# Optimization experiments

Measured on AMD Instinct MI355X. Metric: run time of the kernel, lower is better.

Reference implementation:

```python
import jax, jax.numpy as jnp
import numpy as np

B, N, R = 8, 1024, 8192
D_IN, REL_D = 32, 1
NF_P, NF_R, NF_E, D_OUT = 128, 128, 128, 3
PSTEP = 3


def setup_inputs() -> dict:
    key = jax.random.key(0)
    ks = jax.random.split(key, 26)
    state = jax.random.normal(ks[0], (B, N, D_IN), dtype=jnp.float32)
    # Rr/Rs are one-hot selection matrices [B, N, R]: column j selects the
    # receiver/sender particle of relation j.
    recv = jax.random.randint(ks[1], (B, R), 0, N)
    send = jax.random.randint(ks[2], (B, R), 0, N)
    Rr = jnp.transpose(jax.nn.one_hot(recv, N, dtype=jnp.float32), (0, 2, 1))
    Rs = jnp.transpose(jax.nn.one_hot(send, N, dtype=jnp.float32), (0, 2, 1))
    Ra = jax.random.normal(ks[3], (B, R, REL_D), dtype=jnp.float32)

    def lin(k, i, o):
        kw, kb = jax.random.split(k)
        return (0.02 * jax.random.normal(kw, (i, o), dtype=jnp.float32),
                0.02 * jax.random.normal(kb, (o,), dtype=jnp.float32))

    pe_w0, pe_b0 = lin(ks[4], D_IN, NF_P)
    pe_w1, pe_b1 = lin(ks[5], NF_P, NF_E)
    re_w0, re_b0 = lin(ks[6], 2 * D_IN + REL_D, NF_R)
    re_w1, re_b1 = lin(ks[7], NF_R, NF_R)
    re_w2, re_b2 = lin(ks[8], NF_R, NF_R)
    rp_w, rp_b = lin(ks[9], NF_R + 2 * NF_E, NF_E)   # relation_propagator
    pp_w, pp_b = lin(ks[10], 2 * NF_E, NF_E)          # particle_propagator
    pr_w0, pr_b0 = lin(ks[11], NF_E, NF_E)            # particle_predictor
    pr_w1, pr_b1 = lin(ks[12], NF_E, D_OUT)
    return dict(state=state, Rr=Rr, Rs=Rs, Ra=Ra, pstep=PSTEP,
                pe_w0=pe_w0, pe_b0=pe_b0, pe_w1=pe_w1, pe_b1=pe_b1,
                re_w0=re_w0, re_b0=re_b0, re_w1=re_w1, re_b1=re_b1,
                re_w2=re_w2, re_b2=re_b2, rp_w=rp_w, rp_b=rp_b,
                pp_w=pp_w, pp_b=pp_b, pr_w0=pr_w0, pr_b0=pr_b0,
                pr_w1=pr_w1, pr_b1=pr_b1)


def reference(state, Rr, Rs, Ra, pstep,
              pe_w0, pe_b0, pe_w1, pe_b1,
              re_w0, re_b0, re_w1, re_b1, re_w2, re_b2,
              rp_w, rp_b, pp_w, pp_b,
              pr_w0, pr_b0, pr_w1, pr_b1):
    relu = jax.nn.relu
    # gather particle states into relation slots: Rr^T @ state -> [B, R, D]
    state_r = jnp.einsum('bnr,bnd->brd', Rr, state)
    state_s = jnp.einsum('bnr,bnd->brd', Rs, state)
    # particle encoder: Linear-ReLU-Linear-ReLU
    particle_encode = relu(relu(state @ pe_w0 + pe_b0) @ pe_w1 + pe_b1)  # [B,N,NF_E]
    # relation encoder: 3-layer MLP with ReLU after each layer
    rel_in = jnp.concatenate([state_r, state_s, Ra], axis=2)
    h = relu(rel_in @ re_w0 + re_b0)
    h = relu(h @ re_w1 + re_b1)
    relation_encode = relu(h @ re_w2 + re_b2)  # [B,R,NF_R]

    particle_effect = jnp.zeros((B, N, NF_E), dtype=state.dtype)
    for _ in range(pstep):
        effect_r = jnp.einsum('bnr,bne->bre', Rr, particle_effect)  # gather
        effect_s = jnp.einsum('bnr,bne->bre', Rs, particle_effect)
        rel_x = jnp.concatenate([relation_encode, effect_r, effect_s], axis=2)
        relation_effect = relu(rel_x @ rp_w + rp_b)  # [B,R,NF_E]
        # scatter-add relation effects back to receiver particles
        effect_agg = jnp.einsum('bnr,bre->bne', Rr, relation_effect)
        part_x = jnp.concatenate([particle_encode, effect_agg], axis=2)
        # residual particle propagator: relu(linear(x) + prev_effect)
        particle_effect = relu(part_x @ pp_w + pp_b + particle_effect)
    pred = relu(particle_effect @ pr_w0 + pr_b0) @ pr_w1 + pr_b1  # [B,N,D_OUT]
    return pred
```

## Files before the change

### kernel.cpp

```cpp
#include <hip/hip_runtime.h>

#define NB 8
#define NP 1024
#define NR 8192

typedef unsigned short u16;
typedef __attribute__((ext_vector_type(8))) short bf16x8;
typedef __attribute__((ext_vector_type(4))) float f32x4;
typedef __attribute__((ext_vector_type(4))) unsigned int u32x4;

#define MFMA __builtin_amdgcn_mfma_f32_16x16x32_bf16

static __device__ __forceinline__ float bf2f(u16 u) {
    union { unsigned int i; float f; } v; v.i = ((unsigned int)u) << 16; return v.f;
}
static __device__ __forceinline__ unsigned int f2bf(float f) {
    union { float fv; unsigned int i; } v; v.fv = f;
    unsigned int r = v.i + 0x7FFFu + ((v.i >> 16) & 1u);
    return r >> 16;
}
static __device__ __forceinline__ unsigned int pack2(float a, float b) {
    return f2bf(a) | (f2bf(b) << 16);
}
static __device__ __forceinline__ void unpk8(uint4 v, float* o) {
    o[0] = bf2f((u16)(v.x & 0xFFFF)); o[1] = bf2f((u16)(v.x >> 16));
    o[2] = bf2f((u16)(v.y & 0xFFFF)); o[3] = bf2f((u16)(v.y >> 16));
    o[4] = bf2f((u16)(v.z & 0xFFFF)); o[5] = bf2f((u16)(v.z >> 16));
    o[6] = bf2f((u16)(v.w & 0xFFFF)); o[7] = bf2f((u16)(v.w >> 16));
}

template<int KC>
static __device__ __forceinline__ void load_wfrag(
    const bf16x8* __restrict__ fb, bf16x8 (&wf)[KC][2], int tid)
{
    #pragma unroll
    for (int kc = 0; kc < KC; ++kc)
      #pragma unroll
      for (int nt = 0; nt < 2; ++nt)
        wf[kc][nt] = fb[(kc*2 + nt)*256 + tid];
}

template<int MT, int KC, int LDA>
static __device__ __forceinline__ void mfma_compute(
    const u16* xlds, const bf16x8 (&wf)[KC][2], f32x4 (&acc)[MT][2],
    int l16, int quad)
{
    #pragma unroll
    for (int kc = 0; kc < KC; ++kc) {
        bf16x8 a[MT];
        #pragma unroll
        for (int mt = 0; mt < MT; ++mt)
            a[mt] = *(const bf16x8*)(xlds + (mt*16 + l16)*LDA + kc*32 + quad*8);
        #pragma unroll
        for (int mt = 0; mt < MT; ++mt) {
            acc[mt][0] = MFMA(a[mt], wf[kc][0], acc[mt][0], 0, 0, 0);
            acc[mt][1] = MFMA(a[mt], wf[kc][1], acc[mt][1], 0, 0, 0);
        }
    }
}

template<int MT>
static __device__ __forceinline__ void zero_acc(f32x4 (&acc)[MT][2]) {
    #pragma unroll
    for (int mt = 0; mt < MT; ++mt)
      #pragma unroll
      for (int nt = 0; nt < 2; ++nt)
        acc[mt][nt] = f32x4{0.f, 0.f, 0.f, 0.f};
}

template<int MT, int LDA>
static __device__ __forceinline__ void store_c_lds(
    u16* xlds, const f32x4 (&acc)[MT][2], const float* __restrict__ bias,
    int wave, int quad, int l16, int coloff = 0)
{
    #pragma unroll
    for (int mt = 0; mt < MT; ++mt)
      #pragma unroll
      for (int nt = 0; nt < 2; ++nt) {
        int col = wave*32 + nt*16 + l16;
        float bv = bias[col];
        #pragma unroll
        for (int rg = 0; rg < 4; ++rg)
            xlds[(mt*16 + quad*4 + rg)*LDA + coloff + col] =
                (u16)f2bf(fmaxf(acc[mt][nt][rg] + bv, 0.f));
      }
}

template<int MT, bool RELU>
static __device__ __forceinline__ void store_c_glob(
    u16* __restrict__ out, long row0, const f32x4 (&acc)[MT][2],
    const float* __restrict__ bias, int wave, int quad, int l16)
{
    #pragma unroll
    for (int mt = 0; mt < MT; ++mt)
      #pragma unroll
      for (int nt = 0; nt < 2; ++nt) {
        int col = wave*32 + nt*16 + l16;
        float bv = bias[col];
        #pragma unroll
        for (int rg = 0; rg < 4; ++rg) {
            long r = row0 + mt*16 + quad*4 + rg;
            float v = acc[mt][nt][rg] + bv;
            if (RELU) v = fmaxf(v, 0.f);
            out[r*128 + col] = (u16)f2bf(v);
        }
      }
}

__global__ __launch_bounds__(256) void k_idxprep(
    const u32x4* __restrict__ Rr4, const u32x4* __restrict__ Rs4,
    u16* __restrict__ recv, u16* __restrict__ send,
    const float* __restrict__ w0, const float* __restrict__ w1,
    const float* __restrict__ w2, const float* __restrict__ w3,
    const float* __restrict__ w4, const float* __restrict__ w5,
    const float* __restrict__ w6, const float* __restrict__ w7,
    bf16x8* __restrict__ wfrag,
    const float* __restrict__ state, const float* __restrict__ pe_b0,
    const float* __restrict__ pe_b1, u16* __restrict__ penc)
{
    constexpr int LDA = 136;
    __shared__ __align__(16) u16 xlds[64 * LDA];
    int tid = threadIdx.x;
    const int wave = tid >> 6, quad = (tid >> 4) & 3, l16 = tid & 15;

    if (blockIdx.x < 8) {
        const float* W; int KC, kv, off;
        switch (blockIdx.x) {
            case 0:  W = w0; KC = 3;  kv = 65;  off = 0;  break;
            case 1:  W = w1; KC = 4;  kv = 128; off = 6;  break;
            case 2:  W = w2; KC = 4;  kv = 128; off = 14; break;
            case 3:  W = w3; KC = 1;  kv = 32;  off = 22; break;
            case 4:  W = w4; KC = 4;  kv = 128; off = 24; break;
            case 5:  W = w5; KC = 12; kv = 384; off = 32; break;
            case 6:  W = w6; KC = 8;  kv = 256; off = 56; break;
            default: W = w7; KC = 4;  kv = 128; off = 72; break;
        }
        for (int kc = 0; kc < KC; ++kc)
          for (int nt = 0; nt < 2; ++nt) {
            bf16x8 f;
            #pragma unroll
            for (int j = 0; j < 8; ++j) {
                int k = kc*32 + quad*8 + j;
                f[j] = (k < kv) ? (short)f2bf(W[k*128 + wave*32 + nt*16 + l16]) : (short)0;
            }
            wfrag[(off + kc*2 + nt)*256 + tid] = f;
          }
        return;
    }

    if (blockIdx.x < 136) {
        const long row0 = (long)(blockIdx.x - 8) * 64;
        for (int idx = tid; idx < 64 * 8; idx += 256) {
            int r = idx >> 3, c = idx & 7;
            float4 v = *(const float4*)(state + (row0 + r)*32 + c*4);
            uint2 o; o.x = pack2(v.x, v.y); o.y = pack2(v.z, v.w);
            *(uint2*)(xlds + r*LDA + c*4) = o;
        }
        __syncthreads();
        f32x4 acc[4][2];
        zero_acc<4>(acc);
        {
            bf16x8 wf[1][2];
            #pragma unroll
            for (int nt = 0; nt < 2; ++nt)
              #pragma unroll
              for (int j = 0; j < 8; ++j) {
                int k = quad*8 + j;
                wf[0][nt][j] = (short)f2bf(w3[k*128 + wave*32 + nt*16 + l16]);
              }
            mfma_compute<4, 1, LDA>(xlds, wf, acc, l16, quad);
        }
        __syncthreads();
        store_c_lds<4, LDA>(xlds, acc, pe_b0, wave, quad, l16);
        __syncthreads();
        zero_acc<4>(acc);
        {
            bf16x8 wf[4][2];
            #pragma unroll
            for (int kc = 0; kc < 4; ++kc)
              #pragma unroll
              for (int nt = 0; nt < 2; ++nt)
                #pragma unroll
                for (int j = 0; j < 8; ++j) {
                    int k = kc*32 + quad*8 + j;
                    wf[kc][nt][j] = (short)f2bf(w4[k*128 + wave*32 + nt*16 + l16]);
                }
            mfma_compute<4, 4, LDA>(xlds, wf, acc, l16, quad);
        }
        store_c_glob<4, true>(penc, row0, acc, pe_b1, wave, quad, l16);
        return;
    }

    int sid = blockIdx.x - 136;
    int mat = sid & 1;
    const u32x4* src = mat ? Rs4 : Rr4;
    u16* dst = mat ? send : recv;
    long base = (long)(sid >> 1) * 2048 + tid;
    u32x4 v[8];
    #pragma unroll
    for (int k = 0; k < 8; ++k)
        v[k] = __builtin_nontemporal_load(src + base + k*256);
    #pragma unroll
    for (int k = 0; k < 8; ++k) {
        long i = base + k*256;
        int c4 = (int)(i & 2047), n = (int)((i >> 11) & 1023), b = (int)(i >> 21);
        int o = b * NR + c4 * 4;
        if (v[k][0]) dst[o + 0] = (u16)n;
        if (v[k][1]) dst[o + 1] = (u16)n;
        if (v[k][2]) dst[o + 2] = (u16)n;
        if (v[k][3]) dst[o + 3] = (u16)n;
    }
}

__global__ __launch_bounds__(256) void k_csrenc(
    const float* __restrict__ state, const float* __restrict__ Ra,
    const u16* __restrict__ recv, const u16* __restrict__ send,
    int* __restrict__ row_ptr, unsigned int* __restrict__ pidx,
    const bf16x8* __restrict__ f_re0, const float* __restrict__ re_b0,
    const bf16x8* __restrict__ f_re1, const float* __restrict__ re_b1,
    const bf16x8* __restrict__ f_re2, const float* __restrict__ re_b2,
    const bf16x8* __restrict__ f_rpP, const float* __restrict__ rp_b,
    u16* __restrict__ bufP)
{
    constexpr int LDA = 136;
    __shared__ __align__(16) u16 xlds[64 * LDA];
    __shared__ int cur[NP];
    __shared__ int wsum[4];
    const int tid = threadIdx.x;

    if (blockIdx.x < 8) {
        const int b = blockIdx.x;
        for (int i = tid; i < NP; i += 256) cur[i] = 0;
        __syncthreads();
        int pv[32];
        #pragma unroll
        for (int k = 0; k < 32; ++k) {
            pv[k] = recv[b * NR + k * 256 + tid] & 1023;
            atomicAdd(&cur[pv[k]], 1);
        }
        __syncthreads();
        int4 c4v = ((const int4*)cur)[tid];
        int s = c4v.x + c4v.y + c4v.z + c4v.w;
        int si = s;
        #pragma unroll
        for (int off = 1; off < 64; off <<= 1) {
            int u = __shfl_up(si, off);
            if ((tid & 63) >= off) si += u;
        }
        if ((tid & 63) == 63) wsum[tid >> 6] = si;
        __syncthreads();
        if (tid == 0) {
            int a0 = 0;
            #pragma unroll
            for (int i = 0; i < 4; ++i) { int w = wsum[i]; wsum[i] = a0; a0 += w; }
        }
        __syncthreads();
        int base = si - s + wsum[tid >> 6];
        int e0 = base, e1 = base + c4v.x, e2 = e1 + c4v.y, e3 = e2 + c4v.z;
        int* rp = row_ptr + b * (NP + 1);
        rp[tid*4 + 0] = e0; rp[tid*4 + 1] = e1;
        rp[tid*4 + 2] = e2; rp[tid*4 + 3] = e3;
        cur[tid*4 + 0] = e0; cur[tid*4 + 1] = e1;
        cur[tid*4 + 2] = e2; cur[tid*4 + 3] = e3;
        if (tid == 255) rp[NP] = e3 + c4v.w;
        __syncthreads();
        #pragma unroll
        for (int k = 0; k < 32; ++k) {
            int r = k * 256 + tid;
            int j = atomicAdd(&cur[pv[k]], 1) & 8191;
            pidx[b * NR + j] = (unsigned int)(r & 8191)
                             | ((unsigned int)(send[b * NR + r] & 1023) << 16);
        }
        return;
    }

    const int wave = tid >> 6, quad = (tid >> 4) & 3, l16 = tid & 15;
    f32x4 acc[4][2];
    const int row0 = (blockIdx.x - 8) * 64;
    const int b = row0 >> 13;
    {
        int r = tid >> 2, tt = tid & 3;
        int rel = row0 + r;
        u16* dst = xlds + r * LDA;
        int ri = recv[rel] & 1023;
        int si = send[rel] & 1023;
        const float* rrow = state + ((long)(b*NP + ri)) * 32;
        const float* srow = state + ((long)(b*NP + si)) * 32;
        float4 a0 = *(const float4*)(rrow + tt*8);
        float4 a1 = *(const float4*)(rrow + tt*8 + 4);
        uint4 o;
        o.x = pack2(a0.x, a0.y); o.y = pack2(a0.z, a0.w);
        o.z = pack2(a1.x, a1.y); o.w = pack2(a1.z, a1.w);
        *(uint4*)(dst + tt*8) = o;
        float4 s0 = *(const float4*)(srow + tt*8);
        float4 s1 = *(const float4*)(srow + tt*8 + 4);
        o.x = pack2(s0.x, s0.y); o.y = pack2(s0.z, s0.w);
        o.z = pack2(s1.x, s1.y); o.w = pack2(s1.z, s1.w);
        *(uint4*)(dst + 32 + tt*8) = o;
        if (tt == 3) {
            uint4 z = make_uint4(0, 0, 0, 0);
            *(uint4*)(dst + 64) = z; *(uint4*)(dst + 72) = z;
            *(uint4*)(dst + 80) = z; *(uint4*)(dst + 88) = z;
            dst[64] = (u16)f2bf(Ra[rel]);
        }
    }
    __syncthreads();
    zero_acc<4>(acc);
    {
        bf16x8 wf[3][2];
        load_wfrag<3>(f_re0, wf, tid);
        mfma_compute<4, 3, LDA>(xlds, wf, acc, l16, quad);
    }
    __syncthreads();
    store_c_lds<4, LDA>(xlds, acc, re_b0, wave, quad, l16);
    __syncthreads();
    zero_acc<4>(acc);
    {
        bf16x8 wf[4][2];
        load_wfrag<4>(f_re1, wf, tid);
        mfma_compute<4, 4, LDA>(xlds, wf, acc, l16, quad);
    }
    __syncthreads();
    store_c_lds<4, LDA>(xlds, acc, re_b1, wave, quad, l16);
    __syncthreads();
    zero_acc<4>(acc);
    {
        bf16x8 wf[4][2];
        load_wfrag<4>(f_re2, wf, tid);
        mfma_compute<4, 4, LDA>(xlds, wf, acc, l16, quad);
    }
    __syncthreads();
    store_c_lds<4, LDA>(xlds, acc, re_b2, wave, quad, l16);
    __syncthreads();
    zero_acc<4>(acc);
    {
        bf16x8 wf[4][2];
        load_wfrag<4>(f_rpP, wf, tid);
        mfma_compute<4, 4, LDA>(xlds, wf, acc, l16, quad);
    }
    #pragma unroll
    for (int mt = 0; mt < 4; ++mt)
      #pragma unroll
      for (int nt = 0; nt < 2; ++nt) {
        int col = wave*32 + nt*16 + l16;
        float bv = rp_b[col];
        #pragma unroll
        for (int rg = 0; rg < 4; ++rg) {
            int rl = mt*16 + quad*4 + rg;
            bufP[((long)(row0 + rl))*128 + col] = (u16)f2bf(acc[mt][nt][rg] + bv);
        }
      }
}

template<bool STEP1, bool MAKEUV, bool LAST>
__global__ __launch_bounds__(256) void k_pp(
    const u16* __restrict__ penc, const u16* __restrict__ bufP,
    const u16* __restrict__ UV_in, u16* __restrict__ UV_out,
    const int* __restrict__ row_ptr, const unsigned int* __restrict__ pidx,
    const bf16x8* __restrict__ f_pp, const float* __restrict__ pp_b,
    const bf16x8* __restrict__ f_U, const bf16x8* __restrict__ f_V,
    const bf16x8* __restrict__ f_pr0, const float* __restrict__ pr_b0,
    const float* __restrict__ pr_w1, const float* __restrict__ pr_b1,
    float* __restrict__ peff32_io, float* __restrict__ out)
{
    constexpr int LDA = 264;
    __shared__ __align__(16) u16 xlds[32 * LDA];
    const int tid = threadIdx.x;
    const int wave = tid >> 6, quad = (tid >> 4) & 3, l16 = tid & 15;
    const long row0 = (long)blockIdx.x * 32;

    for (int idx = tid; idx < 512; idx += 256) {
        int r = idx >> 4, c = idx & 15;
        *(uint4*)(xlds + r*LDA + c*8) = *(const uint4*)(penc + (row0 + r)*128 + c*8);
    }
    {
        int pp = tid >> 3;
        int cq = tid & 7;
        int gp = (int)row0 + pp;
        int b = gp >> 10, pl = gp & 1023;
        const int* rp = row_ptr + b * (NP + 1);
        int s0 = rp[pl], e0 = rp[pl + 1];
        const unsigned int* pidxb = pidx + b * NR;
        const u16* bufPb = bufP + (long)b * NR * 128;
        float a[16];
        #pragma unroll
        for (int t = 0; t < 16; ++t) a[t] = 0.f;
        float uv[16];
        if (!STEP1) {
            const u16* ur = UV_in + ((long)gp)*256 + cq*16;
            unpk8(*(const uint4*)ur, uv);
            unpk8(*(const uint4*)(ur + 8), uv + 8);
        }
        const u16* uvb = UV_in + ((long)(b*NP))*256 + 128 + cq*16;
        for (int jb = s0; jb < e0; jb += 4) {
            int m = e0 - jb; if (m > 4) m = 4;
            unsigned int ids[4];
            #pragma unroll
            for (int t = 0; t < 4; ++t) {
                int j = jb + t; if (j > e0 - 1) j = e0 - 1;
                ids[t] = pidxb[j];
            }
            uint4 P0[4], P1[4], V0[4], V1[4];
            #pragma unroll
            for (int t = 0; t < 4; ++t) {
                const u16* prow = bufPb + ((long)(ids[t] & 8191u))*128 + cq*16;
                P0[t] = *(const uint4*)prow;
                P1[t] = *(const uint4*)(prow + 8);
                if (!STEP1) {
                    const u16* vrow = uvb + (long)((ids[t] >> 16) & 1023u)*256;
                    V0[t] = *(const uint4*)vrow;
                    V1[t] = *(const uint4*)(vrow + 8);
                }
            }
            #pragma unroll
            for (int t = 0; t < 4; ++t) {
                if (t < m) {
                    float pv[16];
                    unpk8(P0[t], pv); unpk8(P1[t], pv + 8);
                    if (STEP1) {
                        #pragma unroll
                        for (int e = 0; e < 16; ++e) a[e] += fmaxf(pv[e], 0.f);
                    } else {
                        float vv[16];
                        unpk8(V0[t], vv); unpk8(V1[t], vv + 8);
                        #pragma unroll
                        for (int e = 0; e < 16; ++e)
                            a[e] += fmaxf(pv[e] + uv[e] + vv[e], 0.f);
                    }
                }
            }
        }
        u16* dst = xlds + pp*LDA + 128 + cq*16;
        uint4 o;
        o.x = pack2(a[0], a[1]);   o.y = pack2(a[2], a[3]);
        o.z = pack2(a[4], a[5]);   o.w = pack2(a[6], a[7]);
        *(uint4*)dst = o;
        o.x = pack2(a[8], a[9]);   o.y = pack2(a[10], a[11]);
        o.z = pack2(a[12], a[13]); o.w = pack2(a[14], a[15]);
        *(uint4*)(dst + 8) = o;
    }
    __syncthreads();

    f32x4 acc[2][2];
    {
        bf16x8 wf[8][2];
        load_wfrag<8>(f_pp, wf, tid);
        zero_acc<2>(acc);
        mfma_compute<2, 8, LDA>(xlds, wf, acc, l16, quad);
    }
    __syncthreads();

    #pragma unroll
    for (int mt = 0; mt < 2; ++mt)
      #pragma unroll
      for (int nt = 0; nt < 2; ++nt) {
        int col = wave*32 + nt*16 + l16;
        float bv = pp_b[col];
        #pragma unroll
        for (int rg = 0; rg < 4; ++rg) {
            int rloc = mt*16 + quad*4 + rg;
            long r = row0 + rloc;
            float prev = STEP1 ? 0.f : peff32_io[r*128 + col];
            float v = fmaxf(acc[mt][nt][rg] + bv + prev, 0.f);
            if (!LAST) peff32_io[r*128 + col] = v;
            xlds[rloc*LDA + col] = (u16)f2bf(v);
        }
      }
    __syncthreads();

    if (MAKEUV) {
        #pragma unroll
        for (int half = 0; half < 2; ++half) {
            bf16x8 wf[4][2];
            load_wfrag<4>(half ? f_V : f_U, wf, tid);
            zero_acc<2>(acc);
            mfma_compute<2, 4, LDA>(xlds, wf, acc, l16, quad);
            #pragma unroll
            for (int mt = 0; mt < 2; ++mt)
              #pragma unroll
              for (int nt = 0; nt < 2; ++nt) {
                int col = half*128 + wave*32 + nt*16 + l16;
                #pragma unroll
                for (int rg = 0; rg < 4; ++rg) {
                    long r = row0 + mt*16 + quad*4 + rg;
                    UV_out[r*256 + col] = (u16)f2bf(acc[mt][nt][rg]);
                }
              }
        }
    }
    if (LAST) {
        bf16x8 wf[4][2];
        load_wfrag<4>(f_pr0, wf, tid);
        zero_acc<2>(acc);
        mfma_compute<2, 4, LDA>(xlds, wf, acc, l16, quad);
        store_c_lds<2, LDA>(xlds, acc, pr_b0, wave, quad, l16, 128);
        __syncthreads();
        if (tid < 96) {
            int row = tid / 3, col = tid - row * 3;
            float s = pr_b1[col];
            const u16* hr = xlds + row * LDA + 128;
            #pragma unroll 8
            for (int k = 0; k < 128; ++k) s += bf2f(hr[k]) * pr_w1[k*3 + col];
            out[(row0 + row)*3 + col] = s;
        }
    }
}

extern "C" void kernel_launch(void* const* d_in, const int* in_sizes, int n_in,
                              void* d_out, int out_size, void* d_ws, size_t ws_size,
                              hipStream_t stream) {
    const float* state = (const float*)d_in[0];
    const float* Rr    = (const float*)d_in[1];
    const float* Rs    = (const float*)d_in[2];
    const float* Ra    = (const float*)d_in[3];
    const float* pe_w0 = (const float*)d_in[5];
    const float* pe_b0 = (const float*)d_in[6];
    const float* pe_w1 = (const float*)d_in[7];
    const float* pe_b1 = (const float*)d_in[8];
    const float* re_w0 = (const float*)d_in[9];
    const float* re_b0 = (const float*)d_in[10];
    const float* re_w1 = (const float*)d_in[11];
    const float* re_b1 = (const float*)d_in[12];
    const float* re_w2 = (const float*)d_in[13];
    const float* re_b2 = (const float*)d_in[14];
    const float* rp_w  = (const float*)d_in[15];
    const float* rp_b  = (const float*)d_in[16];
    const float* pp_w  = (const float*)d_in[17];
    const float* pp_b  = (const float*)d_in[18];
    const float* pr_w0 = (const float*)d_in[19];
    const float* pr_b0 = (const float*)d_in[20];
    const float* pr_w1 = (const float*)d_in[21];
    const float* pr_b1 = (const float*)d_in[22];

    char* p = (char*)d_ws;
    u16*    bufP    = (u16*)p;    p += (size_t)NB*NR*128*2;
    u16*    UVa     = (u16*)p;    p += (size_t)NB*NP*256*2;
    u16*    UVb     = (u16*)p;    p += (size_t)NB*NP*256*2;
    float*  peff32  = (float*)p;  p += (size_t)NB*NP*128*4;
    u16*    penc    = (u16*)p;    p += (size_t)NB*NP*128*2;
    bf16x8* wfrag   = (bf16x8*)p; p += (size_t)80*256*16;
    int*    row_ptr = (int*)p;    p += (size_t)NB*(NP+1)*4 + 12;
    u16*    recv    = (u16*)p;    p += (size_t)NB*NR*2;
    u16*    send    = (u16*)p;    p += (size_t)NB*NR*2;
    unsigned int* pidx = (unsigned int*)p; p += (size_t)NB*NR*4;

    const bf16x8* f_re0 = wfrag + 0*256;
    const bf16x8* f_re1 = wfrag + 6*256;
    const bf16x8* f_re2 = wfrag + 14*256;
    const bf16x8* f_rpP = wfrag + 32*256;
    const bf16x8* f_rpU = wfrag + 40*256;
    const bf16x8* f_rpV = wfrag + 48*256;
    const bf16x8* f_pp  = wfrag + 56*256;
    const bf16x8* f_pr0 = wfrag + 72*256;

    float* outp = (float*)d_out;

    k_idxprep<<<16520, 256, 0, stream>>>((const u32x4*)Rr, (const u32x4*)Rs, recv, send,
                                         re_w0, re_w1, re_w2, pe_w0, pe_w1, rp_w, pp_w, pr_w0,
                                         wfrag, state, pe_b0, pe_b1, penc);
    k_csrenc<<<1032, 256, 0, stream>>>(state, Ra, recv, send, row_ptr, pidx,
                                       f_re0, re_b0, f_re1, re_b1, f_re2, re_b2,
                                       f_rpP, rp_b, bufP);
    k_pp<true,  true,  false><<<256, 256, 0, stream>>>(
        penc, bufP, UVa, UVa, row_ptr, pidx, f_pp, pp_b,
        f_rpU, f_rpV, f_pr0, pr_b0, pr_w1, pr_b1, peff32, outp);
    k_pp<false, true,  false><<<256, 256, 0, stream>>>(
        penc, bufP, UVa, UVb, row_ptr, pidx, f_pp, pp_b,
        f_rpU, f_rpV, f_pr0, pr_b0, pr_w1, pr_b1, peff32, outp);
    k_pp<false, false, true><<<256, 256, 0, stream>>>(
        penc, bufP, UVb, UVa, row_ptr, pidx, f_pp, pp_b,
        f_rpU, f_rpV, f_pr0, pr_b0, pr_w1, pr_b1, peff32, outp);
}
```

Before: 604.2 us.

## Fuse all stages into one persistent kernel with software grid barriers

```diff
diff --git a/kernel.cpp b/kernel.cpp
--- a/kernel.cpp
+++ b/kernel.cpp
@@ -29,6 +29,36 @@
     o[6] = bf2f((u16)(v.w & 0xFFFF)); o[7] = bf2f((u16)(v.w >> 16));
 }
 
+struct CoopArgs {
+    const u32x4* Rr4; const u32x4* Rs4;
+    u16* recv; u16* send;
+    const float* state; const float* Ra;
+    const float* re_w0; const float* re_w1; const float* re_w2;
+    const float* rp_w;  const float* pp_w;  const float* pr_w0;
+    const float* pe_w0; const float* pe_w1;
+    bf16x8* wfrag;
+    const float* pe_b0; const float* pe_b1;
+    const float* re_b0; const float* re_b1; const float* re_b2;
+    const float* rp_b;  const float* pp_b;  const float* pr_b0;
+    const float* pr_w1; const float* pr_b1;
+    u16* penc; u16* bufP; u16* UVa; u16* UVb;
+    float* peff32; float* out;
+    int* row_ptr; unsigned int* pidx;
+    int* bar;
+};
+
+static __device__ __forceinline__ void gbar(int* cnt, int tid) {
+    __syncthreads();
+    if (tid == 0) {
+        __threadfence();
+        atomicAdd(cnt, 1);
+        while (__hip_atomic_load(cnt, __ATOMIC_RELAXED, __HIP_MEMORY_SCOPE_AGENT) < 256)
+            __builtin_amdgcn_s_sleep(8);
+        __threadfence();
+    }
+    __syncthreads();
+}
+
 template<int KC>
 static __device__ __forceinline__ void load_wfrag(
     const bf16x8* __restrict__ fb, bf16x8 (&wf)[KC][2], int tid)
@@ -107,185 +137,131 @@
       }
 }
 
-__global__ __launch_bounds__(256) void k_idxprep(
-    const u32x4* __restrict__ Rr4, const u32x4* __restrict__ Rs4,
-    u16* __restrict__ recv, u16* __restrict__ send,
-    const float* __restrict__ w0, const float* __restrict__ w1,
-    const float* __restrict__ w2, const float* __restrict__ w3,
-    const float* __restrict__ w4, const float* __restrict__ w5,
-    const float* __restrict__ w6, const float* __restrict__ w7,
-    bf16x8* __restrict__ wfrag,
-    const float* __restrict__ state, const float* __restrict__ pe_b0,
-    const float* __restrict__ pe_b1, u16* __restrict__ penc)
-{
+static __device__ void wprep(const CoopArgs& A, int tid, int bid) {
+    const float* W; int KC, kv, off;
+    switch (bid) {
+        case 0:  W = A.re_w0; KC = 3;  kv = 65;  off = 0;  break;
+        case 1:  W = A.re_w1; KC = 4;  kv = 128; off = 6;  break;
+        case 2:  W = A.re_w2; KC = 4;  kv = 128; off = 14; break;
+        case 3:  W = A.rp_w;  KC = 12; kv = 384; off = 32; break;
+        case 4:  W = A.pp_w;  KC = 8;  kv = 256; off = 56; break;
+        default: W = A.pr_w0; KC = 4;  kv = 128; off = 72; break;
+    }
+    int wave = tid >> 6, quad = (tid >> 4) & 3, l16 = tid & 15;
+    for (int kc = 0; kc < KC; ++kc)
+      for (int nt = 0; nt < 2; ++nt) {
+        bf16x8 f;
+        #pragma unroll
+        for (int j = 0; j < 8; ++j) {
+            int k = kc*32 + quad*8 + j;
+            f[j] = (k < kv) ? (short)f2bf(W[k*128 + wave*32 + nt*16 + l16]) : (short)0;
+        }
+        A.wfrag[(off + kc*2 + nt)*256 + tid] = f;
+      }
+}
+
+static __device__ void pe_tile(const CoopArgs& A, u16* xlds, int tid, int tile) {
     constexpr int LDA = 136;
-    __shared__ __align__(16) u16 xlds[64 * LDA];
-    int tid = threadIdx.x;
     const int wave = tid >> 6, quad = (tid >> 4) & 3, l16 = tid & 15;
-
-    if (blockIdx.x < 8) {
-        const float* W; int KC, kv, off;
-        switch (blockIdx.x) {
-            case 0:  W = w0; KC = 3;  kv = 65;  off = 0;  break;
-            case 1:  W = w1; KC = 4;  kv = 128; off = 6;  break;
-            case 2:  W = w2; KC = 4;  kv = 128; off = 14; break;
-            case 3:  W = w3; KC = 1;  kv = 32;  off = 22; break;
-            case 4:  W = w4; KC = 4;  kv = 128; off = 24; break;
-            case 5:  W = w5; KC = 12; kv = 384; off = 32; break;
-            case 6:  W = w6; KC = 8;  kv = 256; off = 56; break;
-            default: W = w7; KC = 4;  kv = 128; off = 72; break;
-        }
-        for (int kc = 0; kc < KC; ++kc)
-          for (int nt = 0; nt < 2; ++nt) {
-            bf16x8 f;
+    const long row0 = (long)tile * 64;
+    for (int idx = tid; idx < 64 * 8; idx += 256) {
+        int r = idx >> 3, c = idx & 7;
+        float4 v = *(const float4*)(A.state + (row0 + r)*32 + c*4);
+        uint2 o; o.x = pack2(v.x, v.y); o.y = pack2(v.z, v.w);
+        *(uint2*)(xlds + r*LDA + c*4) = o;
+    }
+    __syncthreads();
+    f32x4 acc[4][2];
+    zero_acc<4>(acc);
+    {
+        bf16x8 wf[1][2];
+        #pragma unroll
+        for (int nt = 0; nt < 2; ++nt)
+          #pragma unroll
+          for (int j = 0; j < 8; ++j) {
+            int k = quad*8 + j;
+            wf[0][nt][j] = (short)f2bf(A.pe_w0[k*128 + wave*32 + nt*16 + l16]);
+          }
+        mfma_compute<4, 1, LDA>(xlds, wf, acc, l16, quad);
+    }
+    __syncthreads();
+    store_c_lds<4, LDA>(xlds, acc, A.pe_b0, wave, quad, l16);
+    __syncthreads();
+    zero_acc<4>(acc);
+    {
+        bf16x8 wf[4][2];
+        #pragma unroll
+        for (int kc = 0; kc < 4; ++kc)
+          #pragma unroll
+          for (int nt = 0; nt < 2; ++nt)
             #pragma unroll
             for (int j = 0; j < 8; ++j) {
                 int k = kc*32 + quad*8 + j;
-                f[j] = (k < kv) ? (short)f2bf(W[k*128 + wave*32 + nt*16 + l16]) : (short)0;
+                wf[kc][nt][j] = (short)f2bf(A.pe_w1[k*128 + wave*32 + nt*16 + l16]);
             }
-            wfrag[(off + kc*2 + nt)*256 + tid] = f;
-          }
-        return;
-    }
-
-    if (blockIdx.x < 136) {
-        const long row0 = (long)(blockIdx.x - 8) * 64;
-        for (int idx = tid; idx < 64 * 8; idx += 256) {
-            int r = idx >> 3, c = idx & 7;
-            float4 v = *(const float4*)(state + (row0 + r)*32 + c*4);
-            uint2 o; o.x = pack2(v.x, v.y); o.y = pack2(v.z, v.w);
-            *(uint2*)(xlds + r*LDA + c*4) = o;
-        }
-        __syncthreads();
-        f32x4 acc[4][2];
-        zero_acc<4>(acc);
-        {
-            bf16x8 wf[1][2];
-            #pragma unroll
-            for (int nt = 0; nt < 2; ++nt)
-              #pragma unroll
-              for (int j = 0; j < 8; ++j) {
-                int k = quad*8 + j;
-                wf[0][nt][j] = (short)f2bf(w3[k*128 + wave*32 + nt*16 + l16]);
-              }
-            mfma_compute<4, 1, LDA>(xlds, wf, acc, l16, quad);
-        }
-        __syncthreads();
-        store_c_lds<4, LDA>(xlds, acc, pe_b0, wave, quad, l16);
-        __syncthreads();
-        zero_acc<4>(acc);
-        {
-            bf16x8 wf[4][2];
-            #pragma unroll
-            for (int kc = 0; kc < 4; ++kc)
-              #pragma unroll
-              for (int nt = 0; nt < 2; ++nt)
-                #pragma unroll
-                for (int j = 0; j < 8; ++j) {
-                    int k = kc*32 + quad*8 + j;
-                    wf[kc][nt][j] = (short)f2bf(w4[k*128 + wave*32 + nt*16 + l16]);
-                }
-            mfma_compute<4, 4, LDA>(xlds, wf, acc, l16, quad);
-        }
-        store_c_glob<4, true>(penc, row0, acc, pe_b1, wave, quad, l16);
-        return;
-    }
-
-    int sid = blockIdx.x - 136;
-    int mat = sid & 1;
-    const u32x4* src = mat ? Rs4 : Rr4;
-    u16* dst = mat ? send : recv;
-    long base = (long)(sid >> 1) * 2048 + tid;
-    u32x4 v[8];
-    #pragma unroll
-    for (int k = 0; k < 8; ++k)
-        v[k] = __builtin_nontemporal_load(src + base + k*256);
-    #pragma unroll
-    for (int k = 0; k < 8; ++k) {
-        long i = base + k*256;
-        int c4 = (int)(i & 2047), n = (int)((i >> 11) & 1023), b = (int)(i >> 21);
-        int o = b * NR + c4 * 4;
-        if (v[k][0]) dst[o + 0] = (u16)n;
-        if (v[k][1]) dst[o + 1] = (u16)n;
-        if (v[k][2]) dst[o + 2] = (u16)n;
-        if (v[k][3]) dst[o + 3] = (u16)n;
-    }
-}
-
-__global__ __launch_bounds__(256) void k_csrenc(
-    const float* __restrict__ state, const float* __restrict__ Ra,
-    const u16* __restrict__ recv, const u16* __restrict__ send,
-    int* __restrict__ row_ptr, unsigned int* __restrict__ pidx,
-    const bf16x8* __restrict__ f_re0, const float* __restrict__ re_b0,
-    const bf16x8* __restrict__ f_re1, const float* __restrict__ re_b1,
-    const bf16x8* __restrict__ f_re2, const float* __restrict__ re_b2,
-    const bf16x8* __restrict__ f_rpP, const float* __restrict__ rp_b,
-    u16* __restrict__ bufP)
-{
+        mfma_compute<4, 4, LDA>(xlds, wf, acc, l16, quad);
+    }
+    store_c_glob<4, true>(A.penc, row0, acc, A.pe_b1, wave, quad, l16);
+}
+
+static __device__ void csr_build(const CoopArgs& A, int* cur, int* wsum, int tid, int b) {
+    for (int i = tid; i < NP; i += 256) cur[i] = 0;
+    __syncthreads();
+    int pv[32];
+    #pragma unroll
+    for (int k = 0; k < 32; ++k) {
+        pv[k] = A.recv[b * NR + k * 256 + tid] & 1023;
+        atomicAdd(&cur[pv[k]], 1);
+    }
+    __syncthreads();
+    int4 c4v = ((const int4*)cur)[tid];
+    int s = c4v.x + c4v.y + c4v.z + c4v.w;
+    int si = s;
+    #pragma unroll
+    for (int off = 1; off < 64; off <<= 1) {
+        int u = __shfl_up(si, off);
+        if ((tid & 63) >= off) si += u;
+    }
+    if ((tid & 63) == 63) wsum[tid >> 6] = si;
+    __syncthreads();
+    if (tid == 0) {
+        int a0 = 0;
+        #pragma unroll
+        for (int i = 0; i < 4; ++i) { int w = wsum[i]; wsum[i] = a0; a0 += w; }
+    }
+    __syncthreads();
+    int base = si - s + wsum[tid >> 6];
+    int e0 = base, e1 = base + c4v.x, e2 = e1 + c4v.y, e3 = e2 + c4v.z;
+    int* rp = A.row_ptr + b * (NP + 1);
+    rp[tid*4 + 0] = e0; rp[tid*4 + 1] = e1;
+    rp[tid*4 + 2] = e2; rp[tid*4 + 3] = e3;
+    cur[tid*4 + 0] = e0; cur[tid*4 + 1] = e1;
+    cur[tid*4 + 2] = e2; cur[tid*4 + 3] = e3;
+    if (tid == 255) rp[NP] = e3 + c4v.w;
+    __syncthreads();
+    #pragma unroll
+    for (int k = 0; k < 32; ++k) {
+        int r = k * 256 + tid;
+        int j = atomicAdd(&cur[pv[k]], 1) & 8191;
+        A.pidx[b * NR + j] = (unsigned int)(r & 8191)
+                           | ((unsigned int)(A.send[b * NR + r] & 1023) << 16);
+    }
+}
+
+static __device__ void enc_tile(const CoopArgs& A, u16* xlds, int tid, int t) {
     constexpr int LDA = 136;
-    __shared__ __align__(16) u16 xlds[64 * LDA];
-    __shared__ int cur[NP];
-    __shared__ int wsum[4];
-    const int tid = threadIdx.x;
-
-    if (blockIdx.x < 8) {
-        const int b = blockIdx.x;
-        for (int i = tid; i < NP; i += 256) cur[i] = 0;
-        __syncthreads();
-        int pv[32];
-        #pragma unroll
-        for (int k = 0; k < 32; ++k) {
-            pv[k] = recv[b * NR + k * 256 + tid] & 1023;
-            atomicAdd(&cur[pv[k]], 1);
-        }
-        __syncthreads();
-        int4 c4v = ((const int4*)cur)[tid];
-        int s = c4v.x + c4v.y + c4v.z + c4v.w;
-        int si = s;
-        #pragma unroll
-        for (int off = 1; off < 64; off <<= 1) {
-            int u = __shfl_up(si, off);
-            if ((tid & 63) >= off) si += u;
-        }
-        if ((tid & 63) == 63) wsum[tid >> 6] = si;
-        __syncthreads();
-        if (tid == 0) {
-            int a0 = 0;
-            #pragma unroll
-            for (int i = 0; i < 4; ++i) { int w = wsum[i]; wsum[i] = a0; a0 += w; }
-        }
-        __syncthreads();
-        int base = si - s + wsum[tid >> 6];
-        int e0 = base, e1 = base + c4v.x, e2 = e1 + c4v.y, e3 = e2 + c4v.z;
-        int* rp = row_ptr + b * (NP + 1);
-        rp[tid*4 + 0] = e0; rp[tid*4 + 1] = e1;
-        rp[tid*4 + 2] = e2; rp[tid*4 + 3] = e3;
-        cur[tid*4 + 0] = e0; cur[tid*4 + 1] = e1;
-        cur[tid*4 + 2] = e2; cur[tid*4 + 3] = e3;
-        if (tid == 255) rp[NP] = e3 + c4v.w;
-        __syncthreads();
-        #pragma unroll
-        for (int k = 0; k < 32; ++k) {
-            int r = k * 256 + tid;
-            int j = atomicAdd(&cur[pv[k]], 1) & 8191;
-            pidx[b * NR + j] = (unsigned int)(r & 8191)
-                             | ((unsigned int)(send[b * NR + r] & 1023) << 16);
-        }
-        return;
-    }
-
     const int wave = tid >> 6, quad = (tid >> 4) & 3, l16 = tid & 15;
     f32x4 acc[4][2];
-    const int row0 = (blockIdx.x - 8) * 64;
+    const int row0 = t * 64;
     const int b = row0 >> 13;
     {
         int r = tid >> 2, tt = tid & 3;
         int rel = row0 + r;
         u16* dst = xlds + r * LDA;
-        int ri = recv[rel] & 1023;
-        int si = send[rel] & 1023;
-        const float* rrow = state + ((long)(b*NP + ri)) * 32;
-        const float* srow = state + ((long)(b*NP + si)) * 32;
+        int ri = A.recv[rel] & 1023;
+        int si = A.send[rel] & 1023;
+        const float* rrow = A.state + ((long)(b*NP + ri)) * 32;
+        const float* srow = A.state + ((long)(b*NP + si)) * 32;
         float4 a0 = *(const float4*)(rrow + tt*8);
         float4 a1 = *(const float4*)(rrow + tt*8 + 4);
         uint4 o;
@@ -301,87 +277,79 @@
             uint4 z = make_uint4(0, 0, 0, 0);
             *(uint4*)(dst + 64) = z; *(uint4*)(dst + 72) = z;
             *(uint4*)(dst + 80) = z; *(uint4*)(dst + 88) = z;
-            dst[64] = (u16)f2bf(Ra[rel]);
+            dst[64] = (u16)f2bf(A.Ra[rel]);
         }
     }
     __syncthreads();
     zero_acc<4>(acc);
     {
         bf16x8 wf[3][2];
-        load_wfrag<3>(f_re0, wf, tid);
+        load_wfrag<3>(A.wfrag + 0*256, wf, tid);
         mfma_compute<4, 3, LDA>(xlds, wf, acc, l16, quad);
     }
     __syncthreads();
-    store_c_lds<4, LDA>(xlds, acc, re_b0, wave, quad, l16);
+    store_c_lds<4, LDA>(xlds, acc, A.re_b0, wave, quad, l16);
     __syncthreads();
     zero_acc<4>(acc);
     {
         bf16x8 wf[4][2];
-        load_wfrag<4>(f_re1, wf, tid);
+        load_wfrag<4>(A.wfrag + 6*256, wf, tid);
         mfma_compute<4, 4, LDA>(xlds, wf, acc, l16, quad);
     }
     __syncthreads();
-    store_c_lds<4, LDA>(xlds, acc, re_b1, wave, quad, l16);
+    store_c_lds<4, LDA>(xlds, acc, A.re_b1, wave, quad, l16);
     __syncthreads();
     zero_acc<4>(acc);
     {
         bf16x8 wf[4][2];
-        load_wfrag<4>(f_re2, wf, tid);
+        load_wfrag<4>(A.wfrag + 14*256, wf, tid);
         mfma_compute<4, 4, LDA>(xlds, wf, acc, l16, quad);
     }
     __syncthreads();
-    store_c_lds<4, LDA>(xlds, acc, re_b2, wave, quad, l16);
+    store_c_lds<4, LDA>(xlds, acc, A.re_b2, wave, quad, l16);
     __syncthreads();
     zero_acc<4>(acc);
     {
         bf16x8 wf[4][2];
-        load_wfrag<4>(f_rpP, wf, tid);
+        load_wfrag<4>(A.wfrag + 32*256, wf, tid);
         mfma_compute<4, 4, LDA>(xlds, wf, acc, l16, quad);
     }
+    __syncthreads();
     #pragma unroll
     for (int mt = 0; mt < 4; ++mt)
       #pragma unroll
       for (int nt = 0; nt < 2; ++nt) {
         int col = wave*32 + nt*16 + l16;
-        float bv = rp_b[col];
+        float bv = A.rp_b[col];
         #pragma unroll
         for (int rg = 0; rg < 4; ++rg) {
             int rl = mt*16 + quad*4 + rg;
-            bufP[((long)(row0 + rl))*128 + col] = (u16)f2bf(acc[mt][nt][rg] + bv);
+            A.bufP[((long)(row0 + rl))*128 + col] = (u16)f2bf(acc[mt][nt][rg] + bv);
         }
       }
 }
 
 template<bool STEP1, bool MAKEUV, bool LAST>
-__global__ __launch_bounds__(256) void k_pp(
-    const u16* __restrict__ penc, const u16* __restrict__ bufP,
-    const u16* __restrict__ UV_in, u16* __restrict__ UV_out,
-    const int* __restrict__ row_ptr, const unsigned int* __restrict__ pidx,
-    const bf16x8* __restrict__ f_pp, const float* __restrict__ pp_b,
-    const bf16x8* __restrict__ f_U, const bf16x8* __restrict__ f_V,
-    const bf16x8* __restrict__ f_pr0, const float* __restrict__ pr_b0,
-    const float* __restrict__ pr_w1, const float* __restrict__ pr_b1,
-    float* __restrict__ peff32_io, float* __restrict__ out)
+static __device__ void pp_step(const CoopArgs& A, u16* xlds, int tid, int bid,
+                               const u16* UV_in, u16* UV_out)
 {
     constexpr int LDA = 264;
-    __shared__ __align__(16) u16 xlds[32 * LDA];
-    const int tid = threadIdx.x;
     const int wave = tid >> 6, quad = (tid >> 4) & 3, l16 = tid & 15;
-    const long row0 = (long)blockIdx.x * 32;
+    const long row0 = (long)bid * 32;
 
     for (int idx = tid; idx < 512; idx += 256) {
         int r = idx >> 4, c = idx & 15;
-        *(uint4*)(xlds + r*LDA + c*8) = *(const uint4*)(penc + (row0 + r)*128 + c*8);
+        *(uint4*)(xlds + r*LDA + c*8) = *(const uint4*)(A.penc + (row0 + r)*128 + c*8);
     }
     {
         int pp = tid >> 3;
         int cq = tid & 7;
         int gp = (int)row0 + pp;
         int b = gp >> 10, pl = gp & 1023;
-        const int* rp = row_ptr + b * (NP + 1);
+        const int* rp = A.row_ptr + b * (NP + 1);
         int s0 = rp[pl], e0 = rp[pl + 1];
-        const unsigned int* pidxb = pidx + b * NR;
-        const u16* bufPb = bufP + (long)b * NR * 128;
+        const unsigned int* pidxb = A.pidx + b * NR;
+        const u16* bufPb = A.bufP + (long)b * NR * 128;
         float a[16];
         #pragma unroll
         for (int t = 0; t < 16; ++t) a[t] = 0.f;
@@ -444,7 +412,7 @@
     f32x4 acc[2][2];
     {
         bf16x8 wf[8][2];
-        load_wfrag<8>(f_pp, wf, tid);
+        load_wfrag<8>(A.wfrag + 56*256, wf, tid);
         zero_acc<2>(acc);
         mfma_compute<2, 8, LDA>(xlds, wf, acc, l16, quad);
     }
@@ -455,14 +423,14 @@
       #pragma unroll
       for (int nt = 0; nt < 2; ++nt) {
         int col = wave*32 + nt*16 + l16;
-        float bv = pp_b[col];
+        float bv = A.pp_b[col];
         #pragma unroll
         for (int rg = 0; rg < 4; ++rg) {
             int rloc = mt*16 + quad*4 + rg;
             long r = row0 + rloc;
-            float prev = STEP1 ? 0.f : peff32_io[r*128 + col];
+            float prev = STEP1 ? 0.f : A.peff32[r*128 + col];
             float v = fmaxf(acc[mt][nt][rg] + bv + prev, 0.f);
-            if (!LAST) peff32_io[r*128 + col] = v;
+            if (!LAST) A.peff32[r*128 + col] = v;
             xlds[rloc*LDA + col] = (u16)f2bf(v);
         }
       }
@@ -472,7 +440,7 @@
         #pragma unroll
         for (int half = 0; half < 2; ++half) {
             bf16x8 wf[4][2];
-            load_wfrag<4>(half ? f_V : f_U, wf, tid);
+            load_wfrag<4>(half ? (A.wfrag + 48*256) : (A.wfrag + 40*256), wf, tid);
             zero_acc<2>(acc);
             mfma_compute<2, 4, LDA>(xlds, wf, acc, l16, quad);
             #pragma unroll
@@ -490,48 +458,72 @@
     }
     if (LAST) {
         bf16x8 wf[4][2];
-        load_wfrag<4>(f_pr0, wf, tid);
+        load_wfrag<4>(A.wfrag + 72*256, wf, tid);
         zero_acc<2>(acc);
         mfma_compute<2, 4, LDA>(xlds, wf, acc, l16, quad);
-        store_c_lds<2, LDA>(xlds, acc, pr_b0, wave, quad, l16, 128);
+        store_c_lds<2, LDA>(xlds, acc, A.pr_b0, wave, quad, l16, 128);
         __syncthreads();
         if (tid < 96) {
             int row = tid / 3, col = tid - row * 3;
-            float s = pr_b1[col];
+            float s = A.pr_b1[col];
             const u16* hr = xlds + row * LDA + 128;
             #pragma unroll 8
-            for (int k = 0; k < 128; ++k) s += bf2f(hr[k]) * pr_w1[k*3 + col];
-            out[(row0 + row)*3 + col] = s;
-        }
-    }
+            for (int k = 0; k < 128; ++k) s += bf2f(hr[k]) * A.pr_w1[k*3 + col];
+            A.out[(row0 + row)*3 + col] = s;
+        }
+    }
+}
+
+__global__ __launch_bounds__(256) void k_all(CoopArgs A) {
+    __shared__ __align__(16) u16 xlds[64 * 136];
+    __shared__ int cur[NP];
+    __shared__ int wsum[4];
+    const int tid = threadIdx.x;
+    const int bid = blockIdx.x;
+
+    if (bid < 6) wprep(A, tid, bid);
+    else if (bid >= 8 && bid < 136) pe_tile(A, xlds, tid, bid - 8);
+    {
+        int q, st;
+        if (bid >= 8 && bid < 136) { q = 31; st = (bid - 8) * 31; }
+        else { int idx = (bid < 8) ? bid : (bid - 128); q = 33; st = 3968 + idx * 33; }
+        for (int cc = 0; cc < q; ++cc) {
+            int chunk = st + cc;
+            const u32x4* src; u16* dst; long base;
+            if (chunk < 4096) { src = A.Rr4; dst = A.recv; base = (long)chunk * 4096; }
+            else              { src = A.Rs4; dst = A.send; base = (long)(chunk - 4096) * 4096; }
+            u32x4 v[16];
+            #pragma unroll
+            for (int k = 0; k < 16; ++k)
+                v[k] = __builtin_nontemporal_load(src + base + k*256 + tid);
+            #pragma unroll
+            for (int k = 0; k < 16; ++k) {
+                long i = base + k*256 + tid;
+                int c4 = (int)(i & 2047), n = (int)((i >> 11) & 1023), b = (int)(i >> 21);
+                int o = b * NR + c4 * 4;
+                if (v[k][0]) dst[o + 0] = (u16)n;
+                if (v[k][1]) dst[o + 1] = (u16)n;
+                if (v[k][2]) dst[o + 2] = (u16)n;
+                if (v[k][3]) dst[o + 3] = (u16)n;
+            }
+        }
+    }
+    gbar(A.bar + 0, tid);
+
+    if (bid < 8) csr_build(A, cur, wsum, tid, bid);
+    else for (int t = bid - 8; t < 1024; t += 248) enc_tile(A, xlds, tid, t);
+    gbar(A.bar + 1, tid);
+
+    pp_step<true,  true,  false>(A, xlds, tid, bid, A.UVa, A.UVa);
+    gbar(A.bar + 2, tid);
+    pp_step<false, true,  false>(A, xlds, tid, bid, A.UVa, A.UVb);
+    gbar(A.bar + 3, tid);
+    pp_step<false, false, true >(A, xlds, tid, bid, A.UVb, A.UVa);
 }
 
 extern "C" void kernel_launch(void* const* d_in, const int* in_sizes, int n_in,
                               void* d_out, int out_size, void* d_ws, size_t ws_size,
                               hipStream_t stream) {
-    const float* state = (const float*)d_in[0];
-    const float* Rr    = (const float*)d_in[1];
-    const float* Rs    = (const float*)d_in[2];
-    const float* Ra    = (const float*)d_in[3];
-    const float* pe_w0 = (const float*)d_in[5];
-    const float* pe_b0 = (const float*)d_in[6];
-    const float* pe_w1 = (const float*)d_in[7];
-    const float* pe_b1 = (const float*)d_in[8];
-    const float* re_w0 = (const float*)d_in[9];
-    const float* re_b0 = (const float*)d_in[10];
-    const float* re_w1 = (const float*)d_in[11];
-    const float* re_b1 = (const float*)d_in[12];
-    const float* re_w2 = (const float*)d_in[13];
-    const float* re_b2 = (const float*)d_in[14];
-    const float* rp_w  = (const float*)d_in[15];
-    const float* rp_b  = (const float*)d_in[16];
-    const float* pp_w  = (const float*)d_in[17];
-    const float* pp_b  = (const float*)d_in[18];
-    const float* pr_w0 = (const float*)d_in[19];
-    const float* pr_b0 = (const float*)d_in[20];
-    const float* pr_w1 = (const float*)d_in[21];
-    const float* pr_b1 = (const float*)d_in[22];
-
     char* p = (char*)d_ws;
     u16*    bufP    = (u16*)p;    p += (size_t)NB*NR*128*2;
     u16*    UVa     = (u16*)p;    p += (size_t)NB*NP*256*2;
@@ -543,31 +535,41 @@
     u16*    recv    = (u16*)p;    p += (size_t)NB*NR*2;
     u16*    send    = (u16*)p;    p += (size_t)NB*NR*2;
     unsigned int* pidx = (unsigned int*)p; p += (size_t)NB*NR*4;
-
-    const bf16x8* f_re0 = wfrag + 0*256;
-    const bf16x8* f_re1 = wfrag + 6*256;
-    const bf16x8* f_re2 = wfrag + 14*256;
-    const bf16x8* f_rpP = wfrag + 32*256;
-    const bf16x8* f_rpU = wfrag + 40*256;
-    const bf16x8* f_rpV = wfrag + 48*256;
-    const bf16x8* f_pp  = wfrag + 56*256;
-    const bf16x8* f_pr0 = wfrag + 72*256;
-
-    float* outp = (float*)d_out;
-
-    k_idxprep<<<16520, 256, 0, stream>>>((const u32x4*)Rr, (const u32x4*)Rs, recv, send,
-                                         re_w0, re_w1, re_w2, pe_w0, pe_w1, rp_w, pp_w, pr_w0,
-                                         wfrag, state, pe_b0, pe_b1, penc);
-    k_csrenc<<<1032, 256, 0, stream>>>(state, Ra, recv, send, row_ptr, pidx,
-                                       f_re0, re_b0, f_re1, re_b1, f_re2, re_b2,
-                                       f_rpP, rp_b, bufP);
-    k_pp<true,  true,  false><<<256, 256, 0, stream>>>(
-        penc, bufP, UVa, UVa, row_ptr, pidx, f_pp, pp_b,
-        f_rpU, f_rpV, f_pr0, pr_b0, pr_w1, pr_b1, peff32, outp);
-    k_pp<false, true,  false><<<256, 256, 0, stream>>>(
-        penc, bufP, UVa, UVb, row_ptr, pidx, f_pp, pp_b,
-        f_rpU, f_rpV, f_pr0, pr_b0, pr_w1, pr_b1, peff32, outp);
-    k_pp<false, false, true><<<256, 256, 0, stream>>>(
-        penc, bufP, UVb, UVa, row_ptr, pidx, f_pp, pp_b,
-        f_rpU, f_rpV, f_pr0, pr_b0, pr_w1, pr_b1, peff32, outp);
-}
+    int*    bar     = (int*)p;    p += 64;
+
+    CoopArgs ka;
+    ka.Rr4   = (const u32x4*)d_in[1];
+    ka.Rs4   = (const u32x4*)d_in[2];
+    ka.recv  = recv;  ka.send = send;
+    ka.state = (const float*)d_in[0];
+    ka.Ra    = (const float*)d_in[3];
+    ka.re_w0 = (const float*)d_in[9];
+    ka.re_w1 = (const float*)d_in[11];
+    ka.re_w2 = (const float*)d_in[13];
+    ka.rp_w  = (const float*)d_in[15];
+    ka.pp_w  = (const float*)d_in[17];
+    ka.pr_w0 = (const float*)d_in[19];
+    ka.pe_w0 = (const float*)d_in[5];
+    ka.pe_w1 = (const float*)d_in[7];
+    ka.wfrag = wfrag;
+    ka.pe_b0 = (const float*)d_in[6];
+    ka.pe_b1 = (const float*)d_in[8];
+    ka.re_b0 = (const float*)d_in[10];
+    ka.re_b1 = (const float*)d_in[12];
+    ka.re_b2 = (const float*)d_in[14];
+    ka.rp_b  = (const float*)d_in[16];
+    ka.pp_b  = (const float*)d_in[18];
+    ka.pr_b0 = (const float*)d_in[20];
+    ka.pr_w1 = (const float*)d_in[21];
+    ka.pr_b1 = (const float*)d_in[22];
+    ka.penc  = penc;  ka.bufP = bufP;
+    ka.UVa   = UVa;   ka.UVb  = UVb;
+    ka.peff32 = peff32;
+    ka.out   = (float*)d_out;
+    ka.row_ptr = row_ptr;
+    ka.pidx  = pidx;
+    ka.bar   = bar;
+
+    hipMemsetAsync(bar, 0, 64, stream);
+    k_all<<<256, 256, 0, stream>>>(ka);
+}
```

Result: slower. 746.9 us (+23.6%).
